# Kernel optimization log

Measured on AMD Instinct MI355X. Metric: run time of the kernel, lower is better.

The kernel has to match this reference:

```python
import jax, jax.numpy as jnp
import numpy as np

FEAT_STRIDE = 16
ANCHOR_SCALES = (8.0, 16.0, 32.0)
ANCHOR_RATIOS = (0.5, 1.0, 2.0)
NUM_ANCHORS = 9
PRE_NMS_TOP_N = 12000
POST_NMS_TOP_N = 300
NMS_THRESH = 0.7
POOLING_SIZE = 7
RPN_NEG_OVERLAP = 0.3
RPN_POS_OVERLAP = 0.7


def _generate_base_anchors(base_size=16):
    ratios = np.array(ANCHOR_RATIOS)
    scales = np.array(ANCHOR_SCALES)
    ctr = (base_size - 1) / 2.0
    size = float(base_size * base_size)
    ws = np.round(np.sqrt(size / ratios))
    hs = np.round(ws * ratios)
    ws = (ws[:, None] * scales[None, :]).ravel()  # order (ratio, scale)
    hs = (hs[:, None] * scales[None, :]).ravel()
    return np.stack([ctr - 0.5 * (ws - 1), ctr - 0.5 * (hs - 1),
                     ctr + 0.5 * (ws - 1), ctr + 0.5 * (hs - 1)], axis=1)


def _all_anchors(H, W):
    base = _generate_base_anchors()  # (A,4)
    sx = np.arange(W) * FEAT_STRIDE
    sy = np.arange(H) * FEAT_STRIDE
    sx, sy = np.meshgrid(sx, sy)  # (H,W)
    shifts = np.stack([sx.ravel(), sy.ravel(), sx.ravel(), sy.ravel()], axis=1)  # (H*W,4)
    anchors = (shifts[:, None, :] + base[None, :, :]).reshape(-1, 4)  # order (h,w,a)
    return jnp.asarray(anchors, dtype=jnp.float32)


def _conv(x, w, b):
    y = jax.lax.conv_general_dilated(x, w, (1, 1), 'SAME',
                                     dimension_numbers=('NCHW', 'OIHW', 'NCHW'))
    return y + b[None, :, None, None]


def _decode(anchors, deltas):
    w = anchors[:, 2] - anchors[:, 0] + 1.0
    h = anchors[:, 3] - anchors[:, 1] + 1.0
    cx = anchors[:, 0] + 0.5 * w
    cy = anchors[:, 1] + 0.5 * h
    pcx = deltas[:, 0] * w + cx
    pcy = deltas[:, 1] * h + cy
    pw = jnp.exp(deltas[:, 2]) * w
    ph = jnp.exp(deltas[:, 3]) * h
    return jnp.stack([pcx - 0.5 * pw, pcy - 0.5 * ph, pcx + 0.5 * pw, pcy + 0.5 * ph], axis=1)


def _encode(ex, gt):
    ew = ex[:, 2] - ex[:, 0] + 1.0
    eh = ex[:, 3] - ex[:, 1] + 1.0
    ecx = ex[:, 0] + 0.5 * ew
    ecy = ex[:, 1] + 0.5 * eh
    gw = gt[:, 2] - gt[:, 0] + 1.0
    gh = gt[:, 3] - gt[:, 1] + 1.0
    gcx = gt[:, 0] + 0.5 * gw
    gcy = gt[:, 1] + 0.5 * gh
    return jnp.stack([(gcx - ecx) / ew, (gcy - ecy) / eh,
                      jnp.log(gw / ew), jnp.log(gh / eh)], axis=1)


def _clip_boxes(b, im_h, im_w):
    return jnp.stack([jnp.clip(b[:, 0], 0.0, im_w - 1.0),
                      jnp.clip(b[:, 1], 0.0, im_h - 1.0),
                      jnp.clip(b[:, 2], 0.0, im_w - 1.0),
                      jnp.clip(b[:, 3], 0.0, im_h - 1.0)], axis=1)


def _iou_matrix(a, b):
    aa = (a[:, 2] - a[:, 0] + 1.0) * (a[:, 3] - a[:, 1] + 1.0)
    ba = (b[:, 2] - b[:, 0] + 1.0) * (b[:, 3] - b[:, 1] + 1.0)
    x1 = jnp.maximum(a[:, None, 0], b[None, :, 0])
    y1 = jnp.maximum(a[:, None, 1], b[None, :, 1])
    x2 = jnp.minimum(a[:, None, 2], b[None, :, 2])
    y2 = jnp.minimum(a[:, None, 3], b[None, :, 3])
    inter = jnp.maximum(x2 - x1 + 1.0, 0.0) * jnp.maximum(y2 - y1 + 1.0, 0.0)
    return inter / (aa[:, None] + ba[None, :] - inter)


def _nms(boxes, thresh, max_out):
    # boxes (N,4) already sorted by score descending; greedy NMS, fixed output size
    areas = (boxes[:, 2] - boxes[:, 0] + 1.0) * (boxes[:, 3] - boxes[:, 1] + 1.0)
    N = boxes.shape[0]

    def body(i, state):
        valid, keep = state
        idx = jnp.argmax(valid)  # first still-valid (highest score)
        has = valid[idx]
        b = boxes[idx]
        xx1 = jnp.maximum(b[0], boxes[:, 0])
        yy1 = jnp.maximum(b[1], boxes[:, 1])
        xx2 = jnp.minimum(b[2], boxes[:, 2])
        yy2 = jnp.minimum(b[3], boxes[:, 3])
        inter = jnp.maximum(xx2 - xx1 + 1.0, 0.0) * jnp.maximum(yy2 - yy1 + 1.0, 0.0)
        iou = inter / (areas[idx] + areas - inter)
        valid = jnp.where(has, valid & (iou <= thresh), valid)
        keep = keep.at[i].set(jnp.where(has, idx, 0).astype(jnp.int32))
        return valid, keep

    valid0 = jnp.ones((N,), dtype=bool)
    keep0 = jnp.zeros((max_out,), dtype=jnp.int32)
    _, keep = jax.lax.fori_loop(0, max_out, body, (valid0, keep0))
    return keep


def _roi_crop(feat, rois, P):
    # affine_grid + grid_sample (align_corners=True, zero padding), matching STRPN.pooling
    C, H, W = feat.shape[1], feat.shape[2], feat.shape[3]
    f = feat[0].reshape(C, H * W)
    R = rois.shape[0]
    x1 = rois[:, 1] / 16.0
    y1 = rois[:, 2] / 16.0
    x2 = rois[:, 3] / 16.0
    y2 = rois[:, 4] / 16.0
    t00 = (x2 - x1) / (W - 1)
    t02 = (x1 + x2 - W + 1) / (W - 1)
    t11 = (y2 - y1) / (H - 1)
    t12 = (y1 + y2 - H + 1) / (H - 1)
    lin = jnp.linspace(-1.0, 1.0, P)
    gx = jnp.broadcast_to(t00[:, None, None] * lin[None, None, :] + t02[:, None, None], (R, P, P))
    gy = jnp.broadcast_to(t11[:, None, None] * lin[None, :, None] + t12[:, None, None], (R, P, P))
    ix = (gx + 1.0) * 0.5 * (W - 1)
    iy = (gy + 1.0) * 0.5 * (H - 1)
    ix0 = jnp.floor(ix)
    iy0 = jnp.floor(iy)
    wx = ix - ix0
    wy = iy - iy0

    def gather(yi, xi, wgt):
        valid = (yi >= 0) & (yi < H) & (xi >= 0) & (xi < W)
        yc = jnp.clip(yi, 0, H - 1).astype(jnp.int32)
        xc = jnp.clip(xi, 0, W - 1).astype(jnp.int32)
        v = f[:, yc * W + xc]  # (C,R,P,P)
        return v * (wgt * valid)[None]

    out = (gather(iy0, ix0, (1 - wy) * (1 - wx)) + gather(iy0, ix0 + 1, (1 - wy) * wx)
           + gather(iy0 + 1, ix0, wy * (1 - wx)) + gather(iy0 + 1, ix0 + 1, wy * wx))
    return jnp.transpose(out, (1, 0, 2, 3))  # (R,C,P,P)


def _anchor_targets(anchors, gt_boxes, im_h, im_w):
    inside = ((anchors[:, 0] >= 0) & (anchors[:, 1] >= 0)
              & (anchors[:, 2] < im_w) & (anchors[:, 3] < im_h))
    ov = _iou_matrix(anchors, gt_boxes[:, :4])
    ov = jnp.where(inside[:, None], ov, -1.0)
    max_ov = ov.max(axis=1)
    argmax = ov.argmax(axis=1)
    gt_max = ov.max(axis=0)  # (G,)
    is_best = (ov == gt_max[None, :]).any(axis=1)
    labels = jnp.full(anchors.shape[:1], -1.0, dtype=jnp.float32)
    labels = jnp.where(inside & (max_ov < RPN_NEG_OVERLAP), 0.0, labels)
    labels = jnp.where(inside & is_best, 1.0, labels)
    labels = jnp.where(inside & (max_ov >= RPN_POS_OVERLAP), 1.0, labels)
    targets = _encode(anchors, gt_boxes[argmax, :4])
    pos = (labels == 1.0)
    ex = (labels >= 0.0)
    n_ex = jnp.maximum(ex.sum(), 1).astype(jnp.float32)
    in_w = pos[:, None].astype(jnp.float32)
    out_w = ex[:, None].astype(jnp.float32) / n_ex
    return labels, targets, in_w, out_w


def _forward(head_features, gt_boxes, im_info, rpn_w, rpn_b, cls_w, cls_b, bbox_w, bbox_b):
    A = NUM_ANCHORS
    H, W = head_features.shape[2], head_features.shape[3]
    anchors = _all_anchors(H, W)  # order (h,w,a)
    rpn = jax.nn.relu(_conv(head_features, rpn_w, rpn_b))
    cls_score = _conv(rpn, cls_w, cls_b)[0]   # (2A,H,W); channel layout cls*A + a
    bbox_pred = _conv(rpn, bbox_w, bbox_b)[0]  # (4A,H,W); channel layout a*4 + coord
    cls2 = cls_score.reshape(2, A, H, W)
    fg = jax.nn.softmax(cls2, axis=0)[1]  # (A,H,W)
    scores = jnp.transpose(fg, (1, 2, 0)).reshape(-1)  # (h,w,a)
    deltas = jnp.transpose(bbox_pred.reshape(A, 4, H, W), (2, 3, 0, 1)).reshape(-1, 4)
    im_h, im_w = im_info[0], im_info[1]
    proposals = _clip_boxes(_decode(anchors, deltas), im_h, im_w)
    _, order = jax.lax.top_k(scores, PRE_NMS_TOP_N)
    props = proposals[order]
    keep = _nms(props, NMS_THRESH, POST_NMS_TOP_N)
    sel = props[keep]
    rois = jnp.concatenate([jnp.zeros((POST_NMS_TOP_N, 1), sel.dtype), sel], axis=1)
    # RPN losses (anchor targets are numpy/constants in the original => stop_gradient)
    labels, tgt, iw, ow = jax.tree_util.tree_map(
        jax.lax.stop_gradient, _anchor_targets(anchors, gt_boxes, im_h, im_w))
    logits = jnp.transpose(cls2, (2, 3, 1, 0)).reshape(-1, 2)  # (h,w,a,2)
    logp = jax.nn.log_softmax(logits, axis=-1)
    mask = (labels >= 0).astype(logp.dtype)
    lbl = jnp.clip(labels, 0.0, 1.0).astype(jnp.int32)
    ce = -jnp.take_along_axis(logp, lbl[:, None], axis=1)[:, 0]
    cls_loss = jnp.sum(ce * mask) / jnp.maximum(mask.sum(), 1.0)
    sigma2 = 9.0  # sigma=3
    diff = iw * (deltas - tgt)
    ad = jnp.abs(diff)
    flag = (ad < 1.0 / sigma2).astype(diff.dtype)
    sl1 = flag * 0.5 * sigma2 * diff * diff + (1.0 - flag) * (ad - 0.5 / sigma2)
    box_loss = jnp.sum(ow * sl1)  # batch=1: sum over dims == mean over batch of per-image sums
    pooled = _roi_crop(head_features, jax.lax.stop_gradient(rois), POOLING_SIZE)
    return pooled, cls_loss, box_loss


def setup_inputs() -> dict:
    key = jax.random.key(0)
    ks = jax.random.split(key, 10)
    head_features = jax.random.normal(ks[0], (1, 1024, 96, 96), jnp.float32)
    G = 8
    x1 = jax.random.uniform(ks[1], (G,), minval=0.0, maxval=1100.0)
    y1 = jax.random.uniform(ks[2], (G,), minval=0.0, maxval=1000.0)
    bw = jax.random.uniform(ks[3], (G,), minval=50.0, maxval=300.0)
    bh = jax.random.uniform(ks[4], (G,), minval=100.0, maxval=450.0)
    gt_boxes = jnp.stack([x1, y1, jnp.minimum(x1 + bw, 1535.0),
                          jnp.minimum(y1 + bh, 1535.0), jnp.ones((G,))], axis=1).astype(jnp.float32)
    im_info = jnp.array([1536.0, 1536.0, 1.0], jnp.float32)
    rpn_w = jax.random.normal(ks[5], (512, 1024, 3, 3), jnp.float32) * 0.01
    rpn_b = jnp.zeros((512,), jnp.float32)
    cls_w = jax.random.normal(ks[6], (18, 512, 1, 1), jnp.float32) * 0.01
    cls_b = jnp.zeros((18,), jnp.float32)
    bbox_w = jax.random.normal(ks[7], (36, 512, 1, 1), jnp.float32) * 0.01
    bbox_b = jnp.zeros((36,), jnp.float32)
    return {"head_features": head_features, "gt_boxes": gt_boxes, "im_info": im_info,
            "rpn_w": rpn_w, "rpn_b": rpn_b, "cls_w": cls_w, "cls_b": cls_b,
            "bbox_w": bbox_w, "bbox_b": bbox_b}


def reference(head_features, gt_boxes, im_info, rpn_w, rpn_b, cls_w, cls_b, bbox_w, bbox_b):
    return _forward(head_features, gt_boxes, im_info, rpn_w, rpn_b, cls_w, cls_b, bbox_w, bbox_b)
```

## Files before the change

kernel.cpp:

```cpp
#include <hip/hip_runtime.h>
#include <stdint.h>

typedef unsigned int u32;
typedef unsigned long long u64;
typedef _Float16 f16x8 __attribute__((ext_vector_type(8)));
typedef float f32x4 __attribute__((ext_vector_type(4)));

#define HF 96
#define HW 9216
#define CIN 1024
#define CMID 512
#define NA 82944
#define PRE 12000
#define POST 300
#define NW 188
#define NBLK 324
#define OUT_POOL (POST*CIN*49)

__device__ __constant__ float BA[9][4] = {
  {-84.f,-40.f,99.f,55.f}, {-176.f,-88.f,191.f,103.f}, {-360.f,-184.f,375.f,199.f},
  {-56.f,-56.f,71.f,71.f}, {-120.f,-120.f,135.f,135.f}, {-248.f,-248.f,263.f,263.f},
  {-36.f,-80.f,51.f,95.f}, {-80.f,-168.f,95.f,183.f},  {-168.f,-344.f,183.f,359.f}
};

__device__ __forceinline__ u32 fkey(float f) {
  u32 u = __float_as_uint(f);
  return (u & 0x80000000u) ? ~u : (u | 0x80000000u);
}

__device__ __forceinline__ void gl_lds16(const void* g, void* l) {
  __builtin_amdgcn_global_load_lds((const __attribute__((address_space(1))) void*)g,
                                   (__attribute__((address_space(3))) void*)l, 16, 0, 0);
}

__global__ void prep_img(const float* __restrict__ feat, f16x8* __restrict__ img)
{
  __shared__ float ls[32][100];
  const int yy = blockIdx.x;
  const int kt = blockIdx.y;
  const int tid = threadIdx.x;
  const int y = yy - 1;
  const bool yok = (unsigned)y < 96u;
  if (yok) {
    for (int e = tid; e < 3072; e += 256) {
      const int ci = e / 96;
      const int x = e - ci * 96;
      ls[ci][x] = feat[(size_t)(kt*32 + ci)*HW + y*96 + x];
    }
  }
  __syncthreads();
  for (int idx = tid; idx < 784; idx += 256) {
    const int col = idx >> 3;
    const int q = idx & 7;
    const int x = col - 1;
    f16x8 val;
#pragma unroll
    for (int i=0;i<8;i++) val[i] = (_Float16)0.f;
    if (yok && (unsigned)x < 96u) {
#pragma unroll
      for (int i=0;i<8;i++) {
        const float v = ls[(q&3)*8 + i][x];
        if (q < 4) val[i] = (_Float16)v;
        else { const _Float16 hi = (_Float16)v; val[i] = (_Float16)((v - (float)hi)*1024.f); }
      }
    }
    const int sw = (col + 2*y) & 7;
    img[(size_t)((kt*98 + yy)*98 + col)*8 + (q ^ sw)] = val;
  }
}

__global__ void prep_w(const float* __restrict__ w, f16x8* __restrict__ wbuf)
{
  const int t = blockIdx.x*256 + threadIdx.x;
  const int co = t & 511;
  const int cic = t >> 9;
  const int kt = cic >> 2;
  const int kg = cic & 3;
  const float* wp = w + (size_t)co*9216 + cic*72;
#pragma unroll
  for (int tap=0; tap<9; ++tap) {
    f16x8 hv, lv;
#pragma unroll
    for (int i=0;i<8;i++) {
      const float v = wp[i*9 + tap] * 64.f;
      const _Float16 hi = (_Float16)v;
      hv[i] = hi;
      lv[i] = (_Float16)((v - (float)hi)*1024.f);
    }
    wbuf[(size_t)(((kt*9 + tap)*2 + 0)*4 + kg)*512 + co] = hv;
    wbuf[(size_t)(((kt*9 + tap)*2 + 1)*4 + kg)*512 + co] = lv;
  }
}

__global__ __launch_bounds__(128, 2) void rpn_conv_mfma(
    const f16x8* __restrict__ img, const f16x8* __restrict__ wbuf,
    const float* __restrict__ bias, float* __restrict__ out)
{
  __shared__ f16x8 in_s[2560];
  const int tid = threadIdx.x;
  const int lane = tid & 63;
  const int wv = tid >> 6;
  const int kgrp = lane >> 4;
  const int ln15 = lane & 15;
  const int x0 = blockIdx.x * 48;
  const int y  = blockIdx.y;
  const int co0 = blockIdx.z * 128 + wv * 64;

  int goff[10];
#pragma unroll
  for (int j=0;j<10;j++) {
    int s = j*128 + tid; if (s > 1199) s = 1199;
    const int row = s / 400;
    const int rem = s - row*400;
    goff[j] = ((y + row)*98 + x0 + (rem>>3))*8 + (rem & 7);
  }
  const int ldst0 = wv*64;

  int keyb[3];
#pragma unroll
  for (int pt=0; pt<3; ++pt) keyb[pt] = x0 + pt*16 + ln15 + 1 + 2*y;

  f32x4 acc1[4][3], acc2[4][3];
#pragma unroll
  for (int c=0;c<4;c++)
#pragma unroll
    for (int pt=0;pt<3;pt++) {
      acc1[c][pt] = (f32x4){0.f,0.f,0.f,0.f};
      acc2[c][pt] = (f32x4){0.f,0.f,0.f,0.f};
    }

  const int wlane = kgrp*512 + co0 + ln15;

#pragma unroll
  for (int j=0;j<10;j++) gl_lds16(img + goff[j], in_s + j*128 + ldst0);
  asm volatile("s_waitcnt vmcnt(0)" ::: "memory");
  __syncthreads();

  for (int kt = 0; kt < 32; ++kt) {
    const int cur = (kt & 1) * 1280;
    if (kt < 31) {
      const f16x8* kb = img + (size_t)(kt+1)*76832;
#pragma unroll
      for (int j=0;j<10;j++) gl_lds16(kb + goff[j], in_s + (1280 - cur) + j*128 + ldst0);
    }
    const f16x8* bs = in_s + cur;
#pragma unroll
    for (int t=0; t<9; ++t) {
      const int dy = t/3 - 1, dx = t%3 - 1;
      f16x8 af[4][2];
#pragma unroll
      for (int h=0;h<2;h++) {
        const size_t wb = (size_t)(((kt*9 + t)*2 + h)*2048) + wlane;
#pragma unroll
        for (int c=0;c<4;c++) af[c][h] = wbuf[wb + c*16];
      }
      f16x8 bf[3][2];
#pragma unroll
      for (int pt=0;pt<3;pt++) {
        const int key = (keyb[pt] + dx + 2*dy) & 7;
        const int base = ((dy+1)*50 + pt*16 + ln15 + dx + 1)*8;
#pragma unroll
        for (int h=0;h<2;h++)
          bf[pt][h] = bs[base + ((h*4 + kgrp) ^ key)];
      }
#pragma unroll
      for (int c=0;c<4;c++)
#pragma unroll
        for (int pt=0;pt<3;pt++) {
          acc1[c][pt] = __builtin_amdgcn_mfma_f32_16x16x32_f16(af[c][0], bf[pt][0], acc1[c][pt], 0,0,0);
          acc2[c][pt] = __builtin_amdgcn_mfma_f32_16x16x32_f16(af[c][0], bf[pt][1], acc2[c][pt], 0,0,0);
          acc2[c][pt] = __builtin_amdgcn_mfma_f32_16x16x32_f16(af[c][1], bf[pt][0], acc2[c][pt], 0,0,0);
        }
    }
    asm volatile("s_waitcnt vmcnt(0)" ::: "memory");
    __syncthreads();
  }

  const int pixb = y*96 + x0;
#pragma unroll
  for (int c=0;c<4;c++) {
#pragma unroll
    for (int i=0;i<4;i++) {
      const int co = co0 + c*16 + kgrp*4 + i;
      const float bb = bias[co];
#pragma unroll
      for (int pt=0;pt<3;pt++) {
        const float v = (acc1[c][pt][i] + acc2[c][pt][i]*(1.f/1024.f))*(1.f/64.f) + bb;
        out[(size_t)co*HW + pixb + pt*16 + ln15] = v > 0.f ? v : 0.f;
      }
    }
  }
}

__global__ void conv1x1p(const float* __restrict__ rpn,
    const float* __restrict__ cw, const float* __restrict__ bw,
    float* __restrict__ partial)
{
  const int hw = blockIdx.x * 256 + threadIdx.x;
  const int cg = blockIdx.y;
  const int ci0 = cg * 64;
  float accA[18], accB[36];
#pragma unroll
  for (int c=0;c<18;c++) accA[c]=0.f;
#pragma unroll
  for (int c=0;c<36;c++) accB[c]=0.f;
  for (int ci=ci0; ci<ci0+64; ++ci) {
    const float v = rpn[(size_t)ci*HW + hw];
#pragma unroll
    for (int c=0;c<18;c++) accA[c] = fmaf(v, cw[c*CMID+ci], accA[c]);
#pragma unroll
    for (int c=0;c<36;c++) accB[c] = fmaf(v, bw[c*CMID+ci], accB[c]);
  }
  float* p = partial + (size_t)cg*54*HW;
#pragma unroll
  for (int c=0;c<18;c++) p[(size_t)c*HW + hw] = accA[c];
#pragma unroll
  for (int c=0;c<36;c++) p[(size_t)(18+c)*HW + hw] = accB[c];
}

__global__ void conv1x1r(const float* __restrict__ partial,
    const float* __restrict__ cb, const float* __restrict__ bb,
    float* __restrict__ cls_out, float* __restrict__ bbox_out)
{
  const int o = blockIdx.x*256 + threadIdx.x;
  const int c = o / HW;
  const int hw = o - c*HW;
  float v = partial[o];
#pragma unroll
  for (int g=1; g<8; ++g) v += partial[(size_t)g*54*HW + o];
  if (c < 18) cls_out[(size_t)c*HW + hw] = v + cb[c];
  else        bbox_out[(size_t)(c-18)*HW + hw] = v + bb[c-18];
}

__global__ void score_decode_ov(const float* __restrict__ cls_out,
    const float* __restrict__ bbox_out, const float* __restrict__ im_info,
    const float* __restrict__ gt,
    u64* __restrict__ keys, float4* __restrict__ props, u32* __restrict__ hist10,
    float* __restrict__ ov, u32* __restrict__ gtmax)
{
#pragma clang fp contract(off)
  __shared__ u32 h[1024];
  __shared__ u32 lmax[8];
  const int tid = threadIdx.x;
  for (int i=tid;i<1024;i+=256) h[i]=0;
  if (tid < 8) lmax[tid] = 0u;
  __syncthreads();
  const int n = blockIdx.x*256 + tid;
  const int hw = n / 9;
  const int a  = n - hw*9;
  const int x = hw % HF, y = hw / HF;
  const float l0 = cls_out[a*HW + hw];
  const float l1 = cls_out[(9+a)*HW + hw];
  const float m = fmaxf(l0, l1);
  const float e0 = expf(l0 - m), e1 = expf(l1 - m);
  const float s = e1 / (e0 + e1);
  const u32 sb = __float_as_uint(s);
  keys[n] = ((u64)(~sb) << 32) | (u32)n;
  atomicAdd(&h[sb >> 22], 1u);

  const float ax1 = BA[a][0] + 16.f*(float)x;
  const float ay1 = BA[a][1] + 16.f*(float)y;
  const float ax2 = BA[a][2] + 16.f*(float)x;
  const float ay2 = BA[a][3] + 16.f*(float)y;
  const float aw = ax2 - ax1 + 1.f, ah = ay2 - ay1 + 1.f;
  const float cx = ax1 + 0.5f*aw,  cy = ay1 + 0.5f*ah;
  const float d0 = bbox_out[(a*4+0)*HW + hw];
  const float d1 = bbox_out[(a*4+1)*HW + hw];
  const float d2 = bbox_out[(a*4+2)*HW + hw];
  const float d3 = bbox_out[(a*4+3)*HW + hw];
  const float pcx = d0*aw + cx, pcy = d1*ah + cy;
  const float pw = expf(d2)*aw, ph = expf(d3)*ah;
  const float imh = im_info[0], imw = im_info[1];
  float bx1 = fminf(fmaxf(pcx - 0.5f*pw, 0.f), imw - 1.f);
  float by1 = fminf(fmaxf(pcy - 0.5f*ph, 0.f), imh - 1.f);
  float bx2 = fminf(fmaxf(pcx + 0.5f*pw, 0.f), imw - 1.f);
  float by2 = fminf(fmaxf(pcy + 0.5f*ph, 0.f), imh - 1.f);
  props[n] = make_float4(bx1, by1, bx2, by2);

  const bool inside = (ax1 >= 0.f) && (ay1 >= 0.f) && (ax2 < imw) && (ay2 < imh);
  const float aa = aw * ah;
#pragma unroll
  for (int j=0;j<8;j++) {
    const float g0=gt[j*5+0], g1=gt[j*5+1], g2=gt[j*5+2], g3=gt[j*5+3];
    const float ga = (g2-g0+1.f)*(g3-g1+1.f);
    const float xx1 = fmaxf(ax1,g0), yy1 = fmaxf(ay1,g1);
    const float xx2 = fminf(ax2,g2), yy2 = fminf(ay2,g3);
    const float inter = fmaxf(xx2-xx1+1.f,0.f)*fmaxf(yy2-yy1+1.f,0.f);
    const float iou = inter/(aa+ga-inter);
    const float o = inside ? iou : -1.f;
    ov[(size_t)n*8+j] = o;
    atomicMax(&lmax[j], fkey(o));
  }
  __syncthreads();
  for (int i=tid;i<1024;i+=256) if (h[i]) atomicAdd(&hist10[i], h[i]);
  if (tid < 8) atomicMax(&gtmax[tid], lmax[tid]);
}

__global__ void hist_scan1(const u32* __restrict__ hist10, u32* __restrict__ meta)
{
  __shared__ u32 c[1024];
  const int t = threadIdx.x;
  c[t] = hist10[t];
  __syncthreads();
  if (t == 0) {
    u32 cum = 0;
    int b = 1023;
    for (; b > 0; --b) {
      if (cum + c[b] >= PRE) break;
      cum += c[b];
    }
    meta[0] = (u32)b;
    meta[1] = cum;
  }
}

__global__ void refine_label(const u64* __restrict__ keys, const u32* __restrict__ meta,
                             u32* __restrict__ h64,
                             const float* __restrict__ ov, const u32* __restrict__ gtmax,
                             signed char* __restrict__ labels, signed char* __restrict__ amax,
                             int* __restrict__ exP)
{
  __shared__ u32 h[64];
  __shared__ int se[256];
  const int tid = threadIdx.x;
  if (tid < 64) h[tid] = 0;
  __syncthreads();
  const int n = blockIdx.x*256 + tid;
  const u32 sb = ~(u32)(keys[n] >> 32);
  if ((sb >> 22) == meta[0]) atomicAdd(&h[(sb >> 16) & 63], 1u);

  float best = -3.402823466e38f;
  int arg = 0;
  bool isbest = false;
#pragma unroll
  for (int j=0;j<8;j++) {
    const float o = ov[(size_t)n*8+j];
    if (o > best) { best = o; arg = j; }
    if (fkey(o) == gtmax[j]) isbest = true;
  }
  const bool inside = ov[(size_t)n*8+0] >= 0.f;
  int lab = -1;
  if (inside && best < 0.3f) lab = 0;
  if (inside && isbest) lab = 1;
  if (inside && best >= 0.7f) lab = 1;
  labels[n] = (signed char)lab;
  amax[n] = (signed char)arg;
  se[tid] = (lab >= 0) ? 1 : 0;
  __syncthreads();
  if (tid < 64 && h[tid]) atomicAdd(&h64[tid], h[tid]);
  for (int s=128; s>0; s>>=1) {
    if (tid < s) se[tid] += se[tid+s];
    __syncthreads();
  }
  if (tid==0) exP[blockIdx.x] = se[0];
}

__global__ void hist_scan2(const u32* __restrict__ h64, const u32* __restrict__ meta,
                           u32* __restrict__ thresh)
{
  u32 cum = meta[1];
  int s = 63;
  for (; s > 0; --s) { cum += h64[s]; if (cum >= PRE) break; }
  if (s == 0) cum += h64[0];
  thresh[0] = (meta[0] << 6) | (u32)s;
}

__global__ void collect_loss(const u64* __restrict__ keys, const u32* __restrict__ thresh,
                             u32* __restrict__ counter, u64* __restrict__ cand,
                             const float* __restrict__ cls_out, const float* __restrict__ bbox_out,
                             const float* __restrict__ gt, const signed char* __restrict__ labels,
                             const signed char* __restrict__ amax, float2* __restrict__ lossP)
{
#pragma clang fp contract(off)
  __shared__ float sce[256];
  __shared__ float sbx[256];
  const int tid = threadIdx.x;
  const int n = blockIdx.x*256 + tid;
  const u64 k = keys[n];
  const u32 sb = ~(u32)(k >> 32);
  if ((sb >> 16) >= thresh[0]) {
    u32 p = atomicAdd(counter, 1u);
    cand[p] = k;
  }
  const int hw = n/9, a = n - hw*9;
  const int lab = labels[n];
  float ce = 0.f, bx = 0.f;
  if (lab >= 0) {
    const float l0 = cls_out[a*HW+hw], l1 = cls_out[(9+a)*HW+hw];
    const float m = fmaxf(l0,l1);
    const float lse = m + logf(expf(l0-m)+expf(l1-m));
    ce = lse - (lab==1 ? l1 : l0);
  }
  if (lab == 1) {
    const int x = hw % HF, y = hw / HF;
    const float ax1 = BA[a][0]+16.f*(float)x, ay1 = BA[a][1]+16.f*(float)y;
    const float ax2 = BA[a][2]+16.f*(float)x, ay2 = BA[a][3]+16.f*(float)y;
    const float ew = ax2-ax1+1.f, eh = ay2-ay1+1.f;
    const float ecx = ax1+0.5f*ew, ecy = ay1+0.5f*eh;
    const int g = amax[n];
    const float g0=gt[g*5+0], g1=gt[g*5+1], g2=gt[g*5+2], g3=gt[g*5+3];
    const float gw = g2-g0+1.f, gh = g3-g1+1.f;
    const float gcx = g0+0.5f*gw, gcy = g1+0.5f*gh;
    float tgt[4];
    tgt[0] = (gcx-ecx)/ew;
    tgt[1] = (gcy-ecy)/eh;
    tgt[2] = logf(gw/ew);
    tgt[3] = logf(gh/eh);
#pragma unroll
    for (int j=0;j<4;j++) {
      const float d = bbox_out[(a*4+j)*HW+hw];
      const float diff = d - tgt[j];
      const float ad = fabsf(diff);
      bx += (ad < (1.0f/9.0f)) ? (4.5f*diff*diff) : (ad - 0.5f/9.0f);
    }
  }
  sce[tid]=ce; sbx[tid]=bx;
  __syncthreads();
  for (int s=128;s>0;s>>=1) {
    if (tid<s) { sce[tid]+=sce[tid+s]; sbx[tid]+=sbx[tid+s]; }
    __syncthreads();
  }
  if (tid==0) lossP[blockIdx.x] = make_float2(sce[0], sbx[0]);
}

__global__ void rank_partial(const u64* __restrict__ cand, const u32* __restrict__ counter,
                             u32* __restrict__ rankbuf)
{
  __shared__ u64 sk[256];
  const int M = (int)counter[0];
  if (blockIdx.x*256 >= M) return;
  const int i = blockIdx.x*256 + threadIdx.x;
  const u64 key = (i < M) ? cand[i] : ~0ull;
  const int chunk = ((M + 7)/8 + 255) & ~255;
  const int j0 = blockIdx.y*chunk;
  const int j1 = (j0 + chunk < M) ? (j0 + chunk) : M;
  int rank = 0;
  for (int t0 = j0; t0 < j1; t0 += 256) {
    const int j = t0 + threadIdx.x;
    sk[threadIdx.x] = (j < M) ? cand[j] : ~0ull;
    __syncthreads();
    const int lim = (j1 - t0 < 256) ? (j1 - t0) : 256;
    for (int k=0;k<lim;k++) rank += (sk[k] < key) ? 1 : 0;
    __syncthreads();
  }
  if (i < M && rank) atomicAdd(&rankbuf[i], (u32)rank);
}

__global__ void rank_scatter2(const u64* __restrict__ cand, const u32* __restrict__ counter,
                              const u32* __restrict__ rankbuf, const float4* __restrict__ props,
                              float4* __restrict__ sprops)
{
  const int M = (int)counter[0];
  const int i = blockIdx.x*256 + threadIdx.x;
  if (i >= M) return;
  const u32 r = rankbuf[i];
  if (r < PRE) sprops[r] = props[(u32)cand[i]];
}

__global__ void nms_mask(const float4* __restrict__ sp, u64* __restrict__ mask)
{
#pragma clang fp contract(off)
  if (blockIdx.x*64 + 63 < blockIdx.y*64) return;
  __shared__ float4 cb[64];
  __shared__ float  ca[64];
  const int c0 = blockIdx.x * 64;
  const int cend = min(64, PRE - c0);
  if ((int)threadIdx.x < cend) {
    float4 b = sp[c0 + threadIdx.x];
    cb[threadIdx.x] = b;
    ca[threadIdx.x] = (b.z-b.x+1.f)*(b.w-b.y+1.f);
  }
  __syncthreads();
  const int row = blockIdx.y*64 + threadIdx.x;
  if (row >= PRE) return;
  const float4 rb = sp[row];
  const float ra = (rb.z-rb.x+1.f)*(rb.w-rb.y+1.f);
  u64 bits = 0;
  for (int j=0;j<cend;j++) {
    const float4 c = cb[j];
    const float xx1 = fmaxf(rb.x, c.x), yy1 = fmaxf(rb.y, c.y);
    const float xx2 = fminf(rb.z, c.z), yy2 = fminf(rb.w, c.w);
    const float inter = fmaxf(xx2-xx1+1.f, 0.f) * fmaxf(yy2-yy1+1.f, 0.f);
    const float iou = inter / (ra + ca[j] - inter);
    if (iou > 0.7f) bits |= (1ull << j);
  }
  mask[(size_t)row*NW + blockIdx.x] = bits;
}

__global__ void fused_scan_tr(const u64* __restrict__ mask, const float4* __restrict__ sp,
                              float* __restrict__ rois,
                              const float2* __restrict__ lossP, const int* __restrict__ exP,
                              float* __restrict__ out,
                              const float* __restrict__ feat, float* __restrict__ featT, int doT)
{
  const int b = blockIdx.x;
  if (b == 0) {
    __shared__ int keep_s[POST];
    if (threadIdx.x < 64) {
      const int l = threadIdx.x;
      u64 v[4];
#pragma unroll
      for (int q=0;q<4;q++) {
        const int w = l*4+q;
        u64 val = 0;
        if (w < NW) { val = ~0ull; if (w == NW-1) val = (1ull<<32) - 1ull; }
        v[q] = val;
      }
      for (int it=0; it<POST; ++it) {
        const u64 nz = (v[0]|v[1]) | (v[2]|v[3]);
        const u64 bal = __ballot(nz != 0);
        int idx = -1;
        if (bal != 0) {
          const int src = __ffsll((unsigned long long)bal) - 1;
          int fi = 0;
          if (v[0])      fi = (l*4+0)*64 + __ffsll(v[0]) - 1;
          else if (v[1]) fi = (l*4+1)*64 + __ffsll(v[1]) - 1;
          else if (v[2]) fi = (l*4+2)*64 + __ffsll(v[2]) - 1;
          else if (v[3]) fi = (l*4+3)*64 + __ffsll(v[3]) - 1;
          idx = __shfl(fi, src);
        }
        if (l == 0) keep_s[it] = (idx < 0) ? 0 : idx;
        if (idx >= 0 && nz != 0) {
          const u64* mrow = mask + (size_t)idx*NW + l*4;
          v[0] &= ~mrow[0]; v[1] &= ~mrow[1]; v[2] &= ~mrow[2]; v[3] &= ~mrow[3];
        }
      }
    }
    __syncthreads();
    for (int i = threadIdx.x; i < POST; i += 256) {
      const float4 bb = sp[keep_s[i]];
      rois[i*5+0] = 0.f;
      rois[i*5+1] = bb.x; rois[i*5+2] = bb.y; rois[i*5+3] = bb.z; rois[i*5+4] = bb.w;
    }
  } else if (b == 1) {
    __shared__ float a[256];
    __shared__ float c[256];
    __shared__ int   e[256];
    const int t = threadIdx.x;
    float ax = 0.f, cx = 0.f; int ev = 0;
    if (t < NBLK) { float2 v = lossP[t]; ax = v.x; cx = v.y; ev = exP[t]; }
    if (t + 256 < NBLK) { float2 v = lossP[t+256]; ax += v.x; cx += v.y; ev += exP[t+256]; }
    a[t]=ax; c[t]=cx; e[t]=ev;
    __syncthreads();
    for (int s=128;s>0;s>>=1) {
      if (t<s) { a[t]+=a[t+s]; c[t]+=c[t+s]; e[t]+=e[t+s]; }
      __syncthreads();
    }
    if (t==0) {
      const float nex = (float)max(e[0], 1);
      out[OUT_POOL+0] = a[0] / nex;
      out[OUT_POOL+1] = c[0] / nex;
    }
  } else if (doT) {
    __shared__ float t[64][65];
    const int tt = b - 2;
    const int bxhw = (tt % 144)*64, byc = (tt / 144)*64;
    const int tid = threadIdx.x;
    const int l = tid & 63, g = tid >> 6;
#pragma unroll
    for (int i=0;i<16;i++) {
      const int cL = g + 4*i;
      t[cL][l] = feat[(size_t)(byc+cL)*HW + bxhw + l];
    }
    __syncthreads();
#pragma unroll
    for (int i=0;i<16;i++) {
      const int hwL = g + 4*i;
      featT[(size_t)(bxhw+hwL)*1024 + byc + l] = t[l][hwL];
    }
  }
}

struct __align__(16) Samp { int p0,p1,p2,p3; float w0,w1,w2,w3; };

__device__ __forceinline__ Samp make_samp(const float* __restrict__ rois, int r, int s)
{
#pragma clang fp contract(off)
  const int py = s / 7, px = s - py*7;
  const float x1 = rois[r*5+1] * 0.0625f;
  const float y1 = rois[r*5+2] * 0.0625f;
  const float x2 = rois[r*5+3] * 0.0625f;
  const float y2 = rois[r*5+4] * 0.0625f;
  const float t00 = (x2-x1)/95.f;
  const float t02 = (x1+x2-95.f)/95.f;
  const float t11 = (y2-y1)/95.f;
  const float t12 = (y1+y2-95.f)/95.f;
  const float lx = (float)(px-3)/3.f;
  const float ly = (float)(py-3)/3.f;
  const float gx = t00*lx + t02;
  const float gy = t11*ly + t12;
  const float ix = (gx+1.f)*0.5f*95.f;
  const float iy = (gy+1.f)*0.5f*95.f;
  const float ix0 = floorf(ix), iy0 = floorf(iy);
  const float wx = ix-ix0, wy = iy-iy0;
  const float xs[2] = {ix0, ix0+1.f};
  const float ys[2] = {iy0, iy0+1.f};
  const float wxs[2] = {1.f-wx, wx};
  const float wys[2] = {1.f-wy, wy};
  int pos[4]; float wt[4];
#pragma unroll
  for (int k=0;k<4;k++) {
    const int dy = k>>1, dx = k&1;
    const float yi = ys[dy], xi = xs[dx];
    const bool valid = (yi>=0.f)&&(yi<96.f)&&(xi>=0.f)&&(xi<96.f);
    const int yc = (int)fminf(fmaxf(yi,0.f),95.f);
    const int xc = (int)fminf(fmaxf(xi,0.f),95.f);
    pos[k] = yc*96+xc;
    wt[k] = wys[dy]*wxs[dx] * (valid?1.f:0.f);
  }
  Samp t;
  t.p0=pos[0]; t.p1=pos[1]; t.p2=pos[2]; t.p3=pos[3];
  t.w0=wt[0];  t.w1=wt[1];  t.w2=wt[2];  t.w3=wt[3];
  return t;
}

__global__ void roi_pool_coal(const float* __restrict__ featT, const float* __restrict__ rois,
                              float* __restrict__ out)
{
#pragma clang fp contract(off)
  __shared__ float st[49][257];
  __shared__ Samp sam[49];
  const int tid = threadIdx.x;
  const int r = blockIdx.x, cb = blockIdx.y;
  if (tid < 49) sam[tid] = make_samp(rois, r, tid);
  __syncthreads();
  const int c = cb*256 + tid;
  for (int s=0;s<49;s++) {
    const Samp t = sam[s];
    st[s][tid] = t.w0*featT[(size_t)t.p0*1024+c] + t.w1*featT[(size_t)t.p1*1024+c]
               + t.w2*featT[(size_t)t.p2*1024+c] + t.w3*featT[(size_t)t.p3*1024+c];
  }
  __syncthreads();
  float* ob = out + (size_t)r*50176 + cb*12544;
  for (int i=tid; i<12544; i+=256) {
    const int cL = i / 49, s = i - cL*49;
    ob[i] = st[s][cL];
  }
}

__global__ void roi_pool_gather(const float* __restrict__ feat, const float* __restrict__ rois,
                                float* __restrict__ out)
{
#pragma clang fp contract(off)
  const int o = blockIdx.x*256 + threadIdx.x;
  const int s  = o % 49;
  const int rc = o / 49;
  const int c = rc & (CIN-1);
  const int r = rc >> 10;
  const Samp t = make_samp(rois, r, s);
  const float* f = feat + (size_t)c*HW;
  out[o] = t.w0*f[t.p0] + t.w1*f[t.p1] + t.w2*f[t.p2] + t.w3*f[t.p3];
}

extern "C" void kernel_launch(void* const* d_in, const int* in_sizes, int n_in,
                              void* d_out, int out_size, void* d_ws, size_t ws_size,
                              hipStream_t stream)
{
  const float* feat    = (const float*)d_in[0];
  const float* gt      = (const float*)d_in[1];
  const float* im_info = (const float*)d_in[2];
  const float* rpn_w   = (const float*)d_in[3];
  const float* rpn_b   = (const float*)d_in[4];
  const float* cls_w   = (const float*)d_in[5];
  const float* cls_b   = (const float*)d_in[6];
  const float* bbox_w  = (const float*)d_in[7];
  const float* bbox_b  = (const float*)d_in[8];
  float* out = (float*)d_out;
  char* ws = (char*)d_ws;

  size_t off = 0;
  auto alloc = [&](size_t bytes) {
    size_t o = off;
    off = (off + bytes + 255) & ~(size_t)255;
    return o;
  };
  size_t o_counter = alloc(4);
  size_t o_gtmax   = alloc(32);
  size_t o_thresh  = alloc(4);
  size_t o_meta    = alloc(8);
  size_t o_h64     = alloc(256);
  size_t o_hist10  = alloc(1024*4);
  size_t o_rank    = alloc((size_t)NA*4);
  size_t zeroBytes = off;
  size_t o_cls  = alloc((size_t)18*HW*4);
  size_t o_bbox = alloc((size_t)36*HW*4);
  size_t o_rpn  = alloc((size_t)CMID*HW*4);
  size_t o_R = off;
  const size_t IMG_BYTES  = (size_t)32*98*98*8*16;
  const size_t WBUF_BYTES = (size_t)9*2*128*512*16;
  const size_t FEATT_BYTES= (size_t)HW*1024*4;
  size_t o_img  = o_R;
  size_t o_wbuf = o_R + ((IMG_BYTES + 255) & ~(size_t)255);
  size_t baseC_A = o_R + ((FEATT_BYTES + 255) & ~(size_t)255);
  auto phaseC = [&](size_t base, size_t* offs) {
    size_t co = base;
    auto ca = [&](size_t bytes) { size_t o = co; co = (co + bytes + 255) & ~(size_t)255; return o; };
    offs[0] = ca((size_t)8*54*HW*4);
    co = base;
    offs[1] = ca((size_t)NA*8);
    offs[2] = ca((size_t)NA*16);
    offs[3] = ca((size_t)NA*8);
    offs[4] = ca((size_t)PRE*16);
    offs[5] = ca((size_t)PRE*NW*8);
    offs[6] = ca((size_t)POST*5*4);
    offs[7] = ca((size_t)NA*8*4);
    offs[8] = ca((size_t)NA);
    offs[9] = ca((size_t)NA);
    offs[10]= ca((size_t)NBLK*4);
    offs[11]= ca((size_t)NBLK*8);
    size_t endC = co;
    size_t endB = base + (size_t)8*54*HW*4;
    return endC > endB ? endC : endB;
  };
  size_t offsA[12], offsB[12];
  size_t endA = phaseC(baseC_A, offsA);
  size_t convEnd = o_wbuf + WBUF_BYTES;
  size_t neededA = (endA > convEnd ? endA : convEnd);
  size_t endB = phaseC(o_R, offsB);
  (void)endB;
  const bool useT = (ws_size >= neededA);
  const size_t* offs = useT ? offsA : offsB;
  (void)in_sizes; (void)n_in; (void)out_size;

  hipMemsetAsync(ws, 0, zeroBytes, stream);

  f16x8* img      = (f16x8*)(ws + o_img);
  f16x8* wbuf     = (f16x8*)(ws + o_wbuf);
  float* featT    = (float*)(ws + o_R);
  float* partial  = (float*)(ws + offs[0]);
  float* rpn      = (float*)(ws + o_rpn);
  float* cls_out  = (float*)(ws + o_cls);
  float* bbox_out = (float*)(ws + o_bbox);
  u64*   keys     = (u64*)(ws + offs[1]);
  float4* props   = (float4*)(ws + offs[2]);
  u64*   cand     = (u64*)(ws + offs[3]);
  float4* sprops  = (float4*)(ws + offs[4]);
  u64*   maskp    = (u64*)(ws + offs[5]);
  float* rois     = (float*)(ws + offs[6]);
  float* ovp      = (float*)(ws + offs[7]);
  signed char* labels = (signed char*)(ws + offs[8]);
  signed char* amax   = (signed char*)(ws + offs[9]);
  int*    exP     = (int*)(ws + offs[10]);
  float2* lossP   = (float2*)(ws + offs[11]);
  u32* counter    = (u32*)(ws + o_counter);
  u32* gtmaxp     = (u32*)(ws + o_gtmax);
  u32* thresh     = (u32*)(ws + o_thresh);
  u32* metap      = (u32*)(ws + o_meta);
  u32* h64p       = (u32*)(ws + o_h64);
  u32* hist10     = (u32*)(ws + o_hist10);
  u32* rankbuf    = (u32*)(ws + o_rank);

  prep_img<<<dim3(98,32), 256, 0, stream>>>(feat, img);
  prep_w<<<256, 256, 0, stream>>>(rpn_w, wbuf);
  rpn_conv_mfma<<<dim3(2,96,4), 128, 0, stream>>>(img, wbuf, rpn_b, rpn);
  conv1x1p<<<dim3(36,8), 256, 0, stream>>>(rpn, cls_w, bbox_w, partial);
  conv1x1r<<<54*HW/256, 256, 0, stream>>>(partial, cls_b, bbox_b, cls_out, bbox_out);
  score_decode_ov<<<NBLK, 256, 0, stream>>>(cls_out, bbox_out, im_info, gt,
                                            keys, props, hist10, ovp, gtmaxp);
  hist_scan1<<<1, 1024, 0, stream>>>(hist10, metap);
  refine_label<<<NBLK, 256, 0, stream>>>(keys, metap, h64p, ovp, gtmaxp, labels, amax, exP);
  hist_scan2<<<1, 1, 0, stream>>>(h64p, metap, thresh);
  collect_loss<<<NBLK, 256, 0, stream>>>(keys, thresh, counter, cand,
                                         cls_out, bbox_out, gt, labels, amax, lossP);
  rank_partial<<<dim3(NBLK,8), 256, 0, stream>>>(cand, counter, rankbuf);
  rank_scatter2<<<NBLK, 256, 0, stream>>>(cand, counter, rankbuf, props, sprops);
  nms_mask<<<dim3(NW, NW), 64, 0, stream>>>(sprops, maskp);
  fused_scan_tr<<<2306, 256, 0, stream>>>(maskp, sprops, rois, lossP, exP, out,
                                          feat, featT, useT ? 1 : 0);
  if (useT) roi_pool_coal<<<dim3(POST,4), 256, 0, stream>>>(featT, rois, out);
  else      roi_pool_gather<<<OUT_POOL/256, 256, 0, stream>>>(feat, rois, out);
}
```

Before: 695.8 us.

## Shrink conv tiles, drop LDS double buffering, fold threshold scan into collect

The 3x3 MFMA conv now handles 64 output channels per block instead of 128. It uses a 1D grid where the channel group is the fastest-varying index, so neighbouring blocks share the same input tile in cache. LDS double buffering is removed in favour of a single buffer with load-wait-sync per K step, and launch bounds now target three blocks per SIMD for higher occupancy. The single-thread hist_scan2 kernel is merged into collect_loss: each block recomputes the threshold itself, which saves one launch. The trade-off is less weight reuse per block and exposed load latency, with occupancy expected to hide it.

Result: slower. 850.2 us (+22.2%).

```diff
diff --git a/kernel.cpp b/kernel.cpp
--- a/kernel.cpp
+++ b/kernel.cpp
@@ -92,19 +92,22 @@
   }
 }
 
-__global__ __launch_bounds__(128, 2) void rpn_conv_mfma(
+__global__ __launch_bounds__(128, 3) void rpn_conv_mfma(
     const f16x8* __restrict__ img, const f16x8* __restrict__ wbuf,
     const float* __restrict__ bias, float* __restrict__ out)
 {
-  __shared__ f16x8 in_s[2560];
+  __shared__ f16x8 in_s[1280];
+  const int bid = blockIdx.x;
+  const int cg  = bid & 7;
+  const int seq = bid >> 3;
+  const int x0 = (seq & 1) * 48;
+  const int y  = seq >> 1;
   const int tid = threadIdx.x;
   const int lane = tid & 63;
   const int wv = tid >> 6;
   const int kgrp = lane >> 4;
   const int ln15 = lane & 15;
-  const int x0 = blockIdx.x * 48;
-  const int y  = blockIdx.y;
-  const int co0 = blockIdx.z * 128 + wv * 64;
+  const int co0 = cg * 64 + wv * 32;
 
   int goff[10];
 #pragma unroll
@@ -120,9 +123,9 @@
 #pragma unroll
   for (int pt=0; pt<3; ++pt) keyb[pt] = x0 + pt*16 + ln15 + 1 + 2*y;
 
-  f32x4 acc1[4][3], acc2[4][3];
-#pragma unroll
-  for (int c=0;c<4;c++)
+  f32x4 acc1[2][3], acc2[2][3];
+#pragma unroll
+  for (int c=0;c<2;c++)
 #pragma unroll
     for (int pt=0;pt<3;pt++) {
       acc1[c][pt] = (f32x4){0.f,0.f,0.f,0.f};
@@ -131,28 +134,23 @@
 
   const int wlane = kgrp*512 + co0 + ln15;
 
-#pragma unroll
-  for (int j=0;j<10;j++) gl_lds16(img + goff[j], in_s + j*128 + ldst0);
-  asm volatile("s_waitcnt vmcnt(0)" ::: "memory");
-  __syncthreads();
-
   for (int kt = 0; kt < 32; ++kt) {
-    const int cur = (kt & 1) * 1280;
-    if (kt < 31) {
-      const f16x8* kb = img + (size_t)(kt+1)*76832;
-#pragma unroll
-      for (int j=0;j<10;j++) gl_lds16(kb + goff[j], in_s + (1280 - cur) + j*128 + ldst0);
-    }
-    const f16x8* bs = in_s + cur;
+    __syncthreads();
+    const f16x8* kb = img + (size_t)kt*76832;
+#pragma unroll
+    for (int j=0;j<10;j++) gl_lds16(kb + goff[j], in_s + j*128 + ldst0);
+    asm volatile("s_waitcnt vmcnt(0)" ::: "memory");
+    __syncthreads();
+
 #pragma unroll
     for (int t=0; t<9; ++t) {
       const int dy = t/3 - 1, dx = t%3 - 1;
-      f16x8 af[4][2];
+      f16x8 af[2][2];
 #pragma unroll
       for (int h=0;h<2;h++) {
         const size_t wb = (size_t)(((kt*9 + t)*2 + h)*2048) + wlane;
 #pragma unroll
-        for (int c=0;c<4;c++) af[c][h] = wbuf[wb + c*16];
+        for (int c=0;c<2;c++) af[c][h] = wbuf[wb + c*16];
       }
       f16x8 bf[3][2];
 #pragma unroll
@@ -161,10 +159,10 @@
         const int base = ((dy+1)*50 + pt*16 + ln15 + dx + 1)*8;
 #pragma unroll
         for (int h=0;h<2;h++)
-          bf[pt][h] = bs[base + ((h*4 + kgrp) ^ key)];
+          bf[pt][h] = in_s[base + ((h*4 + kgrp) ^ key)];
       }
 #pragma unroll
-      for (int c=0;c<4;c++)
+      for (int c=0;c<2;c++)
 #pragma unroll
         for (int pt=0;pt<3;pt++) {
           acc1[c][pt] = __builtin_amdgcn_mfma_f32_16x16x32_f16(af[c][0], bf[pt][0], acc1[c][pt], 0,0,0);
@@ -172,13 +170,11 @@
           acc2[c][pt] = __builtin_amdgcn_mfma_f32_16x16x32_f16(af[c][1], bf[pt][0], acc2[c][pt], 0,0,0);
         }
     }
-    asm volatile("s_waitcnt vmcnt(0)" ::: "memory");
-    __syncthreads();
   }
 
   const int pixb = y*96 + x0;
 #pragma unroll
-  for (int c=0;c<4;c++) {
+  for (int c=0;c<2;c++) {
 #pragma unroll
     for (int i=0;i<4;i++) {
       const int co = co0 + c*16 + kgrp*4 + i;
@@ -355,17 +351,8 @@
   if (tid==0) exP[blockIdx.x] = se[0];
 }
 
-__global__ void hist_scan2(const u32* __restrict__ h64, const u32* __restrict__ meta,
-                           u32* __restrict__ thresh)
-{
-  u32 cum = meta[1];
-  int s = 63;
-  for (; s > 0; --s) { cum += h64[s]; if (cum >= PRE) break; }
-  if (s == 0) cum += h64[0];
-  thresh[0] = (meta[0] << 6) | (u32)s;
-}
-
-__global__ void collect_loss(const u64* __restrict__ keys, const u32* __restrict__ thresh,
+__global__ void collect_loss(const u64* __restrict__ keys,
+                             const u32* __restrict__ meta, const u32* __restrict__ h64,
                              u32* __restrict__ counter, u64* __restrict__ cand,
                              const float* __restrict__ cls_out, const float* __restrict__ bbox_out,
                              const float* __restrict__ gt, const signed char* __restrict__ labels,
@@ -374,11 +361,20 @@
 #pragma clang fp contract(off)
   __shared__ float sce[256];
   __shared__ float sbx[256];
+  __shared__ u32 sthr;
   const int tid = threadIdx.x;
+  if (tid == 0) {
+    u32 cum = meta[1];
+    int s = 63;
+    for (; s > 0; --s) { cum += h64[s]; if (cum >= PRE) break; }
+    sthr = (meta[0] << 6) | (u32)s;
+  }
+  __syncthreads();
+  const u32 thr = sthr;
   const int n = blockIdx.x*256 + tid;
   const u64 k = keys[n];
   const u32 sb = ~(u32)(k >> 32);
-  if ((sb >> 16) >= thresh[0]) {
+  if ((sb >> 16) >= thr) {
     u32 p = atomicAdd(counter, 1u);
     cand[p] = k;
   }
@@ -676,7 +672,6 @@
   };
   size_t o_counter = alloc(4);
   size_t o_gtmax   = alloc(32);
-  size_t o_thresh  = alloc(4);
   size_t o_meta    = alloc(8);
   size_t o_h64     = alloc(256);
   size_t o_hist10  = alloc(1024*4);
@@ -744,7 +739,6 @@
   float2* lossP   = (float2*)(ws + offs[11]);
   u32* counter    = (u32*)(ws + o_counter);
   u32* gtmaxp     = (u32*)(ws + o_gtmax);
-  u32* thresh     = (u32*)(ws + o_thresh);
   u32* metap      = (u32*)(ws + o_meta);
   u32* h64p       = (u32*)(ws + o_h64);
   u32* hist10     = (u32*)(ws + o_hist10);
@@ -752,15 +746,14 @@
 
   prep_img<<<dim3(98,32), 256, 0, stream>>>(feat, img);
   prep_w<<<256, 256, 0, stream>>>(rpn_w, wbuf);
-  rpn_conv_mfma<<<dim3(2,96,4), 128, 0, stream>>>(img, wbuf, rpn_b, rpn);
+  rpn_conv_mfma<<<1536, 128, 0, stream>>>(img, wbuf, rpn_b, rpn);
   conv1x1p<<<dim3(36,8), 256, 0, stream>>>(rpn, cls_w, bbox_w, partial);
   conv1x1r<<<54*HW/256, 256, 0, stream>>>(partial, cls_b, bbox_b, cls_out, bbox_out);
   score_decode_ov<<<NBLK, 256, 0, stream>>>(cls_out, bbox_out, im_info, gt,
                                             keys, props, hist10, ovp, gtmaxp);
   hist_scan1<<<1, 1024, 0, stream>>>(hist10, metap);
   refine_label<<<NBLK, 256, 0, stream>>>(keys, metap, h64p, ovp, gtmaxp, labels, amax, exP);
-  hist_scan2<<<1, 1, 0, stream>>>(h64p, metap, thresh);
-  collect_loss<<<NBLK, 256, 0, stream>>>(keys, thresh, counter, cand,
+  collect_loss<<<NBLK, 256, 0, stream>>>(keys, metap, h64p, counter, cand,
                                          cls_out, bbox_out, gt, labels, amax, lossP);
   rank_partial<<<dim3(NBLK,8), 256, 0, stream>>>(cand, counter, rankbuf);
   rank_scatter2<<<NBLK, 256, 0, stream>>>(cand, counter, rankbuf, props, sprops);
```
